# Kernel tuning notes

Hardware: AMD Instinct MI355X
Metric: run time of the kernel (lower is better)

Reference implementation:

```python
import jax, jax.numpy as jnp
import numpy as np

LAYER_START = 4
WIN = 2          # context_window_size (over the LAYER axis)
NORM_EPS = 1e-12 # F.normalize eps
COS_EPS = 1e-8   # cosine_similarity eps


def _alpha_for_k(sf, k, nlay):
    """Alignment/novelty weights for layer k. sf: [B, Ttok, Lay, H].
    Mirrors torch: left = tf[k-w:k] (empty when k<w due to python slicing),
    right = tf[k+1:k+w+1], self row last; QR of window_matrix.T."""
    left = list(range(k - WIN, k)) if k >= WIN else []
    right = list(range(k + 1, min(k + WIN + 1, nlay)))
    rows = left + right + [k]
    m = len(rows)  # 3..5
    W = sf[:, :, jnp.array(rows), :]          # [B,T,m,H]
    A = jnp.swapaxes(W, -1, -2)               # [B,T,H,m]  (window_matrix.T)
    _, R = jnp.linalg.qr(A)                   # reduced: R [B,T,m,m]
    r = R[..., :, -1]                         # [B,T,m]
    Rsub = R[..., :-1, :-1]                   # [B,T,m-1,m-1]
    coln = Rsub / jnp.maximum(jnp.linalg.norm(Rsub, axis=-2, keepdims=True), NORM_EPS)
    row_mean = jnp.mean(coln, axis=-1)        # mean over columns -> [B,T,m-1]
    align = jnp.sum(row_mean * R[..., :-1, -1], axis=-1) / jnp.linalg.norm(r[..., :-1], axis=-1)
    align = 1.0 / (align * m * 2)
    novelty = jnp.abs(r[..., -1]) / jnp.linalg.norm(r, axis=-1)
    return align, novelty


def wk_forward(all_hidden_states, attention_mask):
    # [NL,B,T,H] -> [B, Lay, T, H] after layer_start slice
    emb = jnp.transpose(all_hidden_states, (1, 0, 2, 3))[:, LAYER_START:, :, :]
    B, Lay, T, H = emb.shape
    ntok = T - 1  # attention_mask is all-ones: unmask_num = sum(mask) - 1
    sf = jnp.transpose(emb[:, :, :ntok, :], (0, 2, 1, 3))  # [B,Ttok,Lay,H]
    aligns, novs = [], []
    for k in range(Lay):  # small fixed loop over 9 layers
        a, n = _alpha_for_k(sf, k, Lay)
        aligns.append(a)
        novs.append(n)
    align = jnp.stack(aligns, axis=-1)  # [B,Ttok,Lay]
    nov = jnp.stack(novs, axis=-1)
    align = align / jnp.sum(align, axis=-1, keepdims=True)
    nov = nov / jnp.sum(nov, axis=-1, keepdims=True)
    alpha = align + nov
    alpha = alpha / jnp.sum(alpha, axis=-1, keepdims=True)
    token_emb = jnp.einsum('btl,btlh->bth', alpha, sf)  # unify_token output per token
    # unify_sentence: per-token variance (unbiased) of consecutive-layer cosine sims
    a, b = sf[:, :, 1:, :], sf[:, :, :-1, :]
    num = jnp.sum(a * b, axis=-1)
    den = jnp.maximum(jnp.linalg.norm(a, axis=-1) * jnp.linalg.norm(b, axis=-1), COS_EPS)
    sims = num / den                              # [B,Ttok,Lay-1]
    var_tok = jnp.var(sims, axis=-1, ddof=1)      # torch.var default unbiased
    var_tok = var_tok / jnp.sum(var_tok, axis=-1, keepdims=True)
    return jnp.einsum('bt,bth->bh', var_tok, token_emb)  # [B,H]


def setup_inputs() -> dict:
    key = jax.random.key(0)
    NL, B, T, H = 13, 8, 512, 768
    all_hidden_states = jax.random.normal(key, (NL, B, T, H), dtype=jnp.float32)
    attention_mask = jnp.ones((B, T), dtype=jnp.int32)
    return {"all_hidden_states": all_hidden_states, "attention_mask": attention_mask}


def reference(all_hidden_states, attention_mask):
    return wk_forward(all_hidden_states, attention_mask)
```

## Files before the change

### kernel.cpp

```cpp
#include <hip/hip_runtime.h>
#include <math.h>

#define B_DIM 8
#define T_DIM 512
#define H_DIM 768
#define NTOK 511
#define NLAY 9
#define LAYER_START 4
#define NBAND 35
#define TCHUNK 128

__device__ float g_part[B_DIM * TCHUNK * H_DIM];
__device__ float g_varp[B_DIM * TCHUNK];

#define BOFF(d) ((d)*9 - (d) * ((d)-1) / 2)

template <int CTRL>
__device__ __forceinline__ float dpp_mov(float x) {
  return __builtin_bit_cast(
      float, __builtin_amdgcn_update_dpp(0, __builtin_bit_cast(int, x), CTRL,
                                         0xF, 0xF, true));
}

__device__ __forceinline__ float wave_sum_dpp(float x) {
  x += dpp_mov<0x111>(x);
  x += dpp_mov<0x112>(x);
  x += dpp_mov<0x114>(x);
  x += dpp_mov<0x118>(x);
  x += dpp_mov<0x142>(x);
  x += dpp_mov<0x143>(x);
  return x;
}

__global__ __launch_bounds__(256, 2) void wk_a(const float* __restrict__ ahs) {
  const int chunk = blockIdx.x;
  const int b = blockIdx.y;
  const int wave = threadIdx.x >> 6;
  const int lane = threadIdx.x & 63;
  const int t_raw = chunk * 4 + wave;
  const bool active = (t_raw < NTOK);
  const int t = active ? t_raw : (NTOK - 1);

  __shared__ float sG[4][36];
  __shared__ float lds_out[4][H_DIM];
  __shared__ float lds_var[4];

  const size_t LSTR = (size_t)B_DIM * T_DIM * H_DIM;
  const float* lay0 =
      ahs + (size_t)LAYER_START * LSTR + ((size_t)b * T_DIM + t) * H_DIM;

  float4 v[NLAY][3];
#pragma unroll
  for (int l = 0; l < NLAY; ++l) {
    const float* base = lay0 + (size_t)l * LSTR;
#pragma unroll
    for (int s = 0; s < 3; ++s) {
      v[l][s] = *reinterpret_cast<const float4*>(base + s * 256 + lane * 4);
    }
  }

#pragma unroll
  for (int d = 0; d <= 4; ++d) {
    float gd[NLAY];
#pragma unroll
    for (int i = 0; i + d < NLAY; ++i) {
      float s0 = 0.f;
#pragma unroll
      for (int s = 0; s < 3; ++s) {
        const float4 x = v[i][s], y = v[i + d][s];
        s0 += x.x * y.x + x.y * y.y + x.z * y.z + x.w * y.w;
      }
      gd[i] = s0;
    }
#pragma unroll
    for (int i = 0; i + d < NLAY; ++i) gd[i] = wave_sum_dpp(gd[i]);
    if (lane == 63) {
#pragma unroll
      for (int i = 0; i + d < NLAY; ++i) sG[wave][BOFF(d) + i] = gd[i];
    }
  }
  __builtin_amdgcn_wave_barrier();

  const int k = lane < NLAY ? lane : NLAY - 1;
  const int nl = (k >= 2) ? 2 : 0;
  const int nrr = (NLAY - 1 - k) < 2 ? (NLAY - 1 - k) : 2;
  const int m = nl + nrr + 1;

  auto rowf = [&](int i) -> int {
    return (i < nl) ? (k - 2 + i) : ((i < nl + nrr) ? (k + 1 + i - nl) : k);
  };
  auto GK = [&](int i, int j) -> float {
    int a = rowf(i), c = rowf(j);
    int lo = a < c ? a : c;
    int d = (a < c ? c : a) - lo;
    return sG[wave][d * 9 - d * (d - 1) / 2 + lo];
  };

  float R[5][5];
#pragma unroll
  for (int j = 0; j < 5; ++j)
#pragma unroll
    for (int i = 0; i < 5; ++i) R[i][j] = 0.f;

#pragma unroll
  for (int j = 0; j < 5; ++j) {
    if (j < m) {
#pragma unroll
      for (int i = 0; i < 5; ++i) {
        if (i < j) {
          float s = GK(i, j);
#pragma unroll
          for (int p = 0; p < 4; ++p)
            if (p < i) s -= R[p][i] * R[p][j];
          R[i][j] = s / R[i][i];
        }
      }
      float sjj = GK(j, j);
#pragma unroll
      for (int p = 0; p < 4; ++p)
        if (p < j) sjj -= R[p][j] * R[p][j];
      R[j][j] = sqrtf(fmaxf(sjj, 0.f));
    }
  }

  float r[5];
#pragma unroll
  for (int i = 0; i < 5; ++i)
    r[i] = (m == 3) ? R[i][2] : ((m == 4) ? R[i][3] : R[i][4]);

  float rowmean[4] = {0.f, 0.f, 0.f, 0.f};
#pragma unroll
  for (int j = 0; j < 4; ++j) {
    if (j < m - 1) {
      float cn = 0.f;
#pragma unroll
      for (int i = 0; i < 4; ++i)
        if (i <= j) cn += R[i][j] * R[i][j];
      cn = fmaxf(sqrtf(cn), 1e-12f);
      float inv = 1.f / cn;
#pragma unroll
      for (int i = 0; i < 4; ++i)
        if (i < m - 1) rowmean[i] += R[i][j] * inv;
    }
  }

  const float inv_m1 = 1.f / (float)(m - 1);
  float dotv = 0.f, nrm2 = 0.f;
#pragma unroll
  for (int i = 0; i < 4; ++i) {
    if (i < m - 1) {
      dotv += (rowmean[i] * inv_m1) * r[i];
      nrm2 += r[i] * r[i];
    }
  }
  float align_raw = dotv / sqrtf(nrm2);
  float align_v = 1.f / (align_raw * (float)m * 2.f);
  float rlast = (m == 3) ? r[2] : ((m == 4) ? r[3] : r[4]);
  float nov_v = fabsf(rlast) / sqrtf(nrm2 + rlast * rlast);

  float al[NLAY], nv[NLAY];
  float asum = 0.f, nsum = 0.f;
#pragma unroll
  for (int l = 0; l < NLAY; ++l) {
    al[l] = __shfl(align_v, l, 64);
    nv[l] = __shfl(nov_v, l, 64);
    asum += al[l];
    nsum += nv[l];
  }
  float alpha[NLAY];
  float csum = 0.f;
#pragma unroll
  for (int l = 0; l < NLAY; ++l) {
    alpha[l] = al[l] / asum + nv[l] / nsum;
    csum += alpha[l];
  }
  const float inv_csum = 1.f / csum;

  float sims[NLAY - 1];
  float smean = 0.f;
#pragma unroll
  for (int j = 0; j < NLAY - 1; ++j) {
    float num = sG[wave][BOFF(1) + j];
    float den = fmaxf(sqrtf(sG[wave][j]) * sqrtf(sG[wave][j + 1]), 1e-8f);
    sims[j] = num / den;
    smean += sims[j];
  }
  smean *= (1.f / 8.f);
  float var = 0.f;
#pragma unroll
  for (int j = 0; j < NLAY - 1; ++j) {
    float d = sims[j] - smean;
    var += d * d;
  }
  var *= (1.f / 7.f);
  if (!active) var = 0.f;

  if (lane == 0) lds_var[wave] = var;

  float c[NLAY];
#pragma unroll
  for (int l = 0; l < NLAY; ++l) c[l] = var * alpha[l] * inv_csum;

#pragma unroll
  for (int s = 0; s < 3; ++s) {
    float4 o;
    o.x = 0.f; o.y = 0.f; o.z = 0.f; o.w = 0.f;
#pragma unroll
    for (int l = 0; l < NLAY; ++l) {
      o.x += c[l] * v[l][s].x;
      o.y += c[l] * v[l][s].y;
      o.z += c[l] * v[l][s].z;
      o.w += c[l] * v[l][s].w;
    }
    *reinterpret_cast<float4*>(&lds_out[wave][s * 256 + lane * 4]) = o;
  }
  __syncthreads();

  float* dst = g_part + ((size_t)(b * TCHUNK + chunk)) * H_DIM;
#pragma unroll
  for (int s = 0; s < 3; ++s) {
    int h = s * 256 + threadIdx.x;
    float sum = lds_out[0][h] + lds_out[1][h] + lds_out[2][h] + lds_out[3][h];
    dst[h] = sum;
  }
  if (threadIdx.x == 0) {
    g_varp[b * TCHUNK + chunk] =
        lds_var[0] + lds_var[1] + lds_var[2] + lds_var[3];
  }
}

__global__ __launch_bounds__(256) void wk_r(float* __restrict__ out) {
  const int b = blockIdx.y;
  const int tid = threadIdx.x;
  const int h = blockIdx.x * 256 + tid;

  __shared__ float s_ws[4];
  float vs = (tid < TCHUNK) ? g_varp[b * TCHUNK + tid] : 0.f;
  vs = wave_sum_dpp(vs);
  if ((tid & 63) == 63) s_ws[tid >> 6] = vs;
  __syncthreads();
  const float ssum = s_ws[0] + s_ws[1];

  float acc = 0.f;
#pragma unroll 16
  for (int j = 0; j < TCHUNK; ++j)
    acc += g_part[((size_t)(b * TCHUNK + j)) * H_DIM + h];

  out[b * H_DIM + h] = acc / ssum;
}

extern "C" void kernel_launch(void* const* d_in, const int* in_sizes, int n_in,
                              void* d_out, int out_size, void* d_ws, size_t ws_size,
                              hipStream_t stream) {
  const float* ahs = (const float*)d_in[0];
  float* out = (float*)d_out;
  (void)d_ws; (void)ws_size;

  wk_a<<<dim3(TCHUNK, B_DIM), dim3(256), 0, stream>>>(ahs);
  wk_r<<<dim3(3, B_DIM), dim3(256), 0, stream>>>(out);
}
```

Before: 224.5 us.

## Split each token's hidden dim across two waves to halve per-wave registers

Each token is now handled by a pair of waves, each loading half of the hidden dimension (a float4 plus a float2 per lane per layer). Partial Gram entries are combined through shared memory after a block barrier. Blocks now cover two tokens instead of four, so the grid doubles to 256 chunks and the reduction kernel sums twice as many partials. The aim is lower register pressure and more in-flight memory parallelism, at the cost of a block-wide sync, duplicated QR math in both waves, and more partial-sum traffic.

```diff
diff --git a/kernel.cpp b/kernel.cpp
--- a/kernel.cpp
+++ b/kernel.cpp
@@ -8,10 +8,11 @@
 #define NLAY 9
 #define LAYER_START 4
 #define NBAND 35
-#define TCHUNK 128
-
-__device__ float g_part[B_DIM * TCHUNK * H_DIM];
-__device__ float g_varp[B_DIM * TCHUNK];
+#define CHUNKS 256
+#define HHALF 384
+
+__device__ float g_part[B_DIM * CHUNKS * H_DIM];
+__device__ float g_varp[B_DIM * CHUNKS];
 
 #define BOFF(d) ((d)*9 - (d) * ((d)-1) / 2)
 
@@ -37,26 +38,28 @@
   const int b = blockIdx.y;
   const int wave = threadIdx.x >> 6;
   const int lane = threadIdx.x & 63;
-  const int t_raw = chunk * 4 + wave;
+  const int slot = wave >> 1;
+  const int half = wave & 1;
+  const int pb = wave & ~1;
+  const int t_raw = chunk * 2 + slot;
   const bool active = (t_raw < NTOK);
   const int t = active ? t_raw : (NTOK - 1);
 
   __shared__ float sG[4][36];
-  __shared__ float lds_out[4][H_DIM];
-  __shared__ float lds_var[4];
+  __shared__ float lds_out[2][H_DIM];
+  __shared__ float lds_var[2];
 
   const size_t LSTR = (size_t)B_DIM * T_DIM * H_DIM;
-  const float* lay0 =
-      ahs + (size_t)LAYER_START * LSTR + ((size_t)b * T_DIM + t) * H_DIM;
-
-  float4 v[NLAY][3];
-#pragma unroll
-  for (int l = 0; l < NLAY; ++l) {
-    const float* base = lay0 + (size_t)l * LSTR;
-#pragma unroll
-    for (int s = 0; s < 3; ++s) {
-      v[l][s] = *reinterpret_cast<const float4*>(base + s * 256 + lane * 4);
-    }
+  const float* base0 = ahs + (size_t)LAYER_START * LSTR +
+                       ((size_t)b * T_DIM + t) * H_DIM + half * HHALF;
+
+  float4 v4[NLAY];
+  float2 v2[NLAY];
+#pragma unroll
+  for (int l = 0; l < NLAY; ++l) {
+    const float* base = base0 + (size_t)l * LSTR;
+    v4[l] = *reinterpret_cast<const float4*>(base + lane * 4);
+    v2[l] = *reinterpret_cast<const float2*>(base + 256 + lane * 2);
   }
 
 #pragma unroll
@@ -64,13 +67,10 @@
     float gd[NLAY];
 #pragma unroll
     for (int i = 0; i + d < NLAY; ++i) {
-      float s0 = 0.f;
-#pragma unroll
-      for (int s = 0; s < 3; ++s) {
-        const float4 x = v[i][s], y = v[i + d][s];
-        s0 += x.x * y.x + x.y * y.y + x.z * y.z + x.w * y.w;
-      }
-      gd[i] = s0;
+      const float4 x4 = v4[i], y4 = v4[i + d];
+      const float2 x2 = v2[i], y2 = v2[i + d];
+      gd[i] = x4.x * y4.x + x4.y * y4.y + x4.z * y4.z + x4.w * y4.w +
+              x2.x * y2.x + x2.y * y2.y;
     }
 #pragma unroll
     for (int i = 0; i + d < NLAY; ++i) gd[i] = wave_sum_dpp(gd[i]);
@@ -79,7 +79,9 @@
       for (int i = 0; i + d < NLAY; ++i) sG[wave][BOFF(d) + i] = gd[i];
     }
   }
-  __builtin_amdgcn_wave_barrier();
+  __syncthreads();
+
+  auto SC = [&](int idx) -> float { return sG[pb][idx] + sG[pb + 1][idx]; };
 
   const int k = lane < NLAY ? lane : NLAY - 1;
   const int nl = (k >= 2) ? 2 : 0;
@@ -93,7 +95,7 @@
     int a = rowf(i), c = rowf(j);
     int lo = a < c ? a : c;
     int d = (a < c ? c : a) - lo;
-    return sG[wave][d * 9 - d * (d - 1) / 2 + lo];
+    return SC(d * 9 - d * (d - 1) / 2 + lo);
   };
 
   float R[5][5];
@@ -158,30 +160,27 @@
   float rlast = (m == 3) ? r[2] : ((m == 4) ? r[3] : r[4]);
   float nov_v = fabsf(rlast) / sqrtf(nrm2 + rlast * rlast);
 
-  float al[NLAY], nv[NLAY];
   float asum = 0.f, nsum = 0.f;
 #pragma unroll
   for (int l = 0; l < NLAY; ++l) {
-    al[l] = __shfl(align_v, l, 64);
-    nv[l] = __shfl(nov_v, l, 64);
-    asum += al[l];
-    nsum += nv[l];
-  }
-  float alpha[NLAY];
+    asum += __shfl(align_v, l, 64);
+    nsum += __shfl(nov_v, l, 64);
+  }
+  float c[NLAY];
   float csum = 0.f;
 #pragma unroll
   for (int l = 0; l < NLAY; ++l) {
-    alpha[l] = al[l] / asum + nv[l] / nsum;
-    csum += alpha[l];
-  }
-  const float inv_csum = 1.f / csum;
+    float a = __shfl(align_v, l, 64) / asum + __shfl(nov_v, l, 64) / nsum;
+    c[l] = a;
+    csum += a;
+  }
 
   float sims[NLAY - 1];
   float smean = 0.f;
 #pragma unroll
   for (int j = 0; j < NLAY - 1; ++j) {
-    float num = sG[wave][BOFF(1) + j];
-    float den = fmaxf(sqrtf(sG[wave][j]) * sqrtf(sG[wave][j + 1]), 1e-8f);
+    float num = SC(BOFF(1) + j);
+    float den = fmaxf(sqrtf(SC(j)) * sqrtf(SC(j + 1)), 1e-8f);
     sims[j] = num / den;
     smean += sims[j];
   }
@@ -195,37 +194,38 @@
   var *= (1.f / 7.f);
   if (!active) var = 0.f;
 
-  if (lane == 0) lds_var[wave] = var;
-
-  float c[NLAY];
-#pragma unroll
-  for (int l = 0; l < NLAY; ++l) c[l] = var * alpha[l] * inv_csum;
-
-#pragma unroll
-  for (int s = 0; s < 3; ++s) {
-    float4 o;
-    o.x = 0.f; o.y = 0.f; o.z = 0.f; o.w = 0.f;
-#pragma unroll
-    for (int l = 0; l < NLAY; ++l) {
-      o.x += c[l] * v[l][s].x;
-      o.y += c[l] * v[l][s].y;
-      o.z += c[l] * v[l][s].z;
-      o.w += c[l] * v[l][s].w;
-    }
-    *reinterpret_cast<float4*>(&lds_out[wave][s * 256 + lane * 4]) = o;
-  }
+  if (lane == 0 && half == 0) lds_var[slot] = var;
+
+  const float scale = var / csum;
+#pragma unroll
+  for (int l = 0; l < NLAY; ++l) c[l] *= scale;
+
+  float4 o4;
+  o4.x = 0.f; o4.y = 0.f; o4.z = 0.f; o4.w = 0.f;
+  float2 o2;
+  o2.x = 0.f; o2.y = 0.f;
+#pragma unroll
+  for (int l = 0; l < NLAY; ++l) {
+    o4.x += c[l] * v4[l].x;
+    o4.y += c[l] * v4[l].y;
+    o4.z += c[l] * v4[l].z;
+    o4.w += c[l] * v4[l].w;
+    o2.x += c[l] * v2[l].x;
+    o2.y += c[l] * v2[l].y;
+  }
+  *reinterpret_cast<float4*>(&lds_out[slot][half * HHALF + lane * 4]) = o4;
+  *reinterpret_cast<float2*>(&lds_out[slot][half * HHALF + 256 + lane * 2]) =
+      o2;
   __syncthreads();
 
-  float* dst = g_part + ((size_t)(b * TCHUNK + chunk)) * H_DIM;
+  float* dst = g_part + ((size_t)(b * CHUNKS + chunk)) * H_DIM;
 #pragma unroll
   for (int s = 0; s < 3; ++s) {
     int h = s * 256 + threadIdx.x;
-    float sum = lds_out[0][h] + lds_out[1][h] + lds_out[2][h] + lds_out[3][h];
-    dst[h] = sum;
+    dst[h] = lds_out[0][h] + lds_out[1][h];
   }
   if (threadIdx.x == 0) {
-    g_varp[b * TCHUNK + chunk] =
-        lds_var[0] + lds_var[1] + lds_var[2] + lds_var[3];
+    g_varp[b * CHUNKS + chunk] = lds_var[0] + lds_var[1];
   }
 }
 
@@ -235,16 +235,16 @@
   const int h = blockIdx.x * 256 + tid;
 
   __shared__ float s_ws[4];
-  float vs = (tid < TCHUNK) ? g_varp[b * TCHUNK + tid] : 0.f;
+  float vs = g_varp[b * CHUNKS + tid];
   vs = wave_sum_dpp(vs);
   if ((tid & 63) == 63) s_ws[tid >> 6] = vs;
   __syncthreads();
-  const float ssum = s_ws[0] + s_ws[1];
+  const float ssum = s_ws[0] + s_ws[1] + s_ws[2] + s_ws[3];
 
   float acc = 0.f;
 #pragma unroll 16
-  for (int j = 0; j < TCHUNK; ++j)
-    acc += g_part[((size_t)(b * TCHUNK + j)) * H_DIM + h];
+  for (int j = 0; j < CHUNKS; ++j)
+    acc += g_part[((size_t)(b * CHUNKS + j)) * H_DIM + h];
 
   out[b * H_DIM + h] = acc / ssum;
 }
@@ -256,6 +256,6 @@
   float* out = (float*)d_out;
   (void)d_ws; (void)ws_size;
 
-  wk_a<<<dim3(TCHUNK, B_DIM), dim3(256), 0, stream>>>(ahs);
+  wk_a<<<dim3(CHUNKS, B_DIM), dim3(256), 0, stream>>>(ahs);
   wk_r<<<dim3(3, B_DIM), dim3(256), 0, stream>>>(out);
 }
```

Result: slower. 231.4 us (+3.1%).

## Use one-wave blocks per token and move the cross-token reduction to the final kernel

Applied to the files above, without the earlier changes.

The main kernel now launches one 64-thread block per token instead of 256-thread blocks covering four tokens. It drops the LDS cross-wave sum and __syncthreads, and writes each token's weighted partial vector straight to global memory. Input loads are marked nontemporal. The reduction kernel now uses 1024 threads to sum 511 partials per batch instead of 128. This removes intra-block sync and LDS traffic, but the partial buffer grows about fourfold, adding global write and read traffic for the second kernel.

```diff
diff --git a/kernel.cpp b/kernel.cpp
--- a/kernel.cpp
+++ b/kernel.cpp
@@ -8,10 +8,11 @@
 #define NLAY 9
 #define LAYER_START 4
 #define NBAND 35
-#define TCHUNK 128
-
-__device__ float g_part[B_DIM * TCHUNK * H_DIM];
-__device__ float g_varp[B_DIM * TCHUNK];
+
+typedef float vf4 __attribute__((ext_vector_type(4)));
+
+__device__ float g_part[B_DIM * NTOK * H_DIM];
+__device__ float g_varp[B_DIM * NTOK];
 
 #define BOFF(d) ((d)*9 - (d) * ((d)-1) / 2)
 
@@ -32,30 +33,25 @@
   return x;
 }
 
-__global__ __launch_bounds__(256, 2) void wk_a(const float* __restrict__ ahs) {
-  const int chunk = blockIdx.x;
+__global__ __launch_bounds__(64) void wk_a(const float* __restrict__ ahs) {
+  const int t = blockIdx.x;
   const int b = blockIdx.y;
-  const int wave = threadIdx.x >> 6;
-  const int lane = threadIdx.x & 63;
-  const int t_raw = chunk * 4 + wave;
-  const bool active = (t_raw < NTOK);
-  const int t = active ? t_raw : (NTOK - 1);
-
-  __shared__ float sG[4][36];
-  __shared__ float lds_out[4][H_DIM];
-  __shared__ float lds_var[4];
+  const int lane = threadIdx.x;
+
+  __shared__ float sG[36];
 
   const size_t LSTR = (size_t)B_DIM * T_DIM * H_DIM;
   const float* lay0 =
       ahs + (size_t)LAYER_START * LSTR + ((size_t)b * T_DIM + t) * H_DIM;
 
-  float4 v[NLAY][3];
+  vf4 v[NLAY][3];
 #pragma unroll
   for (int l = 0; l < NLAY; ++l) {
     const float* base = lay0 + (size_t)l * LSTR;
 #pragma unroll
     for (int s = 0; s < 3; ++s) {
-      v[l][s] = *reinterpret_cast<const float4*>(base + s * 256 + lane * 4);
+      v[l][s] = __builtin_nontemporal_load(
+          reinterpret_cast<const vf4*>(base + s * 256 + lane * 4));
     }
   }
 
@@ -67,7 +63,7 @@
       float s0 = 0.f;
 #pragma unroll
       for (int s = 0; s < 3; ++s) {
-        const float4 x = v[i][s], y = v[i + d][s];
+        const vf4 x = v[i][s], y = v[i + d][s];
         s0 += x.x * y.x + x.y * y.y + x.z * y.z + x.w * y.w;
       }
       gd[i] = s0;
@@ -76,7 +72,7 @@
     for (int i = 0; i + d < NLAY; ++i) gd[i] = wave_sum_dpp(gd[i]);
     if (lane == 63) {
 #pragma unroll
-      for (int i = 0; i + d < NLAY; ++i) sG[wave][BOFF(d) + i] = gd[i];
+      for (int i = 0; i + d < NLAY; ++i) sG[BOFF(d) + i] = gd[i];
     }
   }
   __builtin_amdgcn_wave_barrier();
@@ -93,7 +89,7 @@
     int a = rowf(i), c = rowf(j);
     int lo = a < c ? a : c;
     int d = (a < c ? c : a) - lo;
-    return sG[wave][d * 9 - d * (d - 1) / 2 + lo];
+    return sG[d * 9 - d * (d - 1) / 2 + lo];
   };
 
   float R[5][5];
@@ -158,30 +154,27 @@
   float rlast = (m == 3) ? r[2] : ((m == 4) ? r[3] : r[4]);
   float nov_v = fabsf(rlast) / sqrtf(nrm2 + rlast * rlast);
 
-  float al[NLAY], nv[NLAY];
   float asum = 0.f, nsum = 0.f;
 #pragma unroll
   for (int l = 0; l < NLAY; ++l) {
-    al[l] = __shfl(align_v, l, 64);
-    nv[l] = __shfl(nov_v, l, 64);
-    asum += al[l];
-    nsum += nv[l];
-  }
-  float alpha[NLAY];
+    asum += __shfl(align_v, l, 64);
+    nsum += __shfl(nov_v, l, 64);
+  }
+  float c[NLAY];
   float csum = 0.f;
 #pragma unroll
   for (int l = 0; l < NLAY; ++l) {
-    alpha[l] = al[l] / asum + nv[l] / nsum;
-    csum += alpha[l];
-  }
-  const float inv_csum = 1.f / csum;
+    float a = __shfl(align_v, l, 64) / asum + __shfl(nov_v, l, 64) / nsum;
+    c[l] = a;
+    csum += a;
+  }
 
   float sims[NLAY - 1];
   float smean = 0.f;
 #pragma unroll
   for (int j = 0; j < NLAY - 1; ++j) {
-    float num = sG[wave][BOFF(1) + j];
-    float den = fmaxf(sqrtf(sG[wave][j]) * sqrtf(sG[wave][j + 1]), 1e-8f);
+    float num = sG[BOFF(1) + j];
+    float den = fmaxf(sqrtf(sG[j]) * sqrtf(sG[j + 1]), 1e-8f);
     sims[j] = num / den;
     smean += sims[j];
   }
@@ -193,18 +186,15 @@
     var += d * d;
   }
   var *= (1.f / 7.f);
-  if (!active) var = 0.f;
-
-  if (lane == 0) lds_var[wave] = var;
-
-  float c[NLAY];
-#pragma unroll
-  for (int l = 0; l < NLAY; ++l) c[l] = var * alpha[l] * inv_csum;
-
+
+  const float scale = var / csum;
+#pragma unroll
+  for (int l = 0; l < NLAY; ++l) c[l] *= scale;
+
+  float* dst = g_part + ((size_t)(b * NTOK + t)) * H_DIM;
 #pragma unroll
   for (int s = 0; s < 3; ++s) {
-    float4 o;
-    o.x = 0.f; o.y = 0.f; o.z = 0.f; o.w = 0.f;
+    vf4 o = {0.f, 0.f, 0.f, 0.f};
 #pragma unroll
     for (int l = 0; l < NLAY; ++l) {
       o.x += c[l] * v[l][s].x;
@@ -212,41 +202,38 @@
       o.z += c[l] * v[l][s].z;
       o.w += c[l] * v[l][s].w;
     }
-    *reinterpret_cast<float4*>(&lds_out[wave][s * 256 + lane * 4]) = o;
-  }
-  __syncthreads();
-
-  float* dst = g_part + ((size_t)(b * TCHUNK + chunk)) * H_DIM;
-#pragma unroll
-  for (int s = 0; s < 3; ++s) {
-    int h = s * 256 + threadIdx.x;
-    float sum = lds_out[0][h] + lds_out[1][h] + lds_out[2][h] + lds_out[3][h];
-    dst[h] = sum;
-  }
-  if (threadIdx.x == 0) {
-    g_varp[b * TCHUNK + chunk] =
-        lds_var[0] + lds_var[1] + lds_var[2] + lds_var[3];
-  }
-}
-
-__global__ __launch_bounds__(256) void wk_r(float* __restrict__ out) {
+    *reinterpret_cast<vf4*>(dst + s * 256 + lane * 4) = o;
+  }
+  if (lane == 0) g_varp[b * NTOK + t] = var;
+}
+
+__global__ __launch_bounds__(1024) void wk_r(float* __restrict__ out) {
   const int b = blockIdx.y;
-  const int tid = threadIdx.x;
+  const int grp = threadIdx.x >> 8;
+  const int tid = threadIdx.x & 255;
   const int h = blockIdx.x * 256 + tid;
 
-  __shared__ float s_ws[4];
-  float vs = (tid < TCHUNK) ? g_varp[b * TCHUNK + tid] : 0.f;
+  __shared__ float s_ws[16];
+  __shared__ float s_acc[4][256];
+
+  float vs = (threadIdx.x < NTOK) ? g_varp[b * NTOK + threadIdx.x] : 0.f;
   vs = wave_sum_dpp(vs);
-  if ((tid & 63) == 63) s_ws[tid >> 6] = vs;
-  __syncthreads();
-  const float ssum = s_ws[0] + s_ws[1];
+  if ((threadIdx.x & 63) == 63) s_ws[threadIdx.x >> 6] = vs;
 
   float acc = 0.f;
 #pragma unroll 16
-  for (int j = 0; j < TCHUNK; ++j)
-    acc += g_part[((size_t)(b * TCHUNK + j)) * H_DIM + h];
-
-  out[b * H_DIM + h] = acc / ssum;
+  for (int j = grp; j < NTOK; j += 4)
+    acc += g_part[((size_t)(b * NTOK + j)) * H_DIM + h];
+  s_acc[grp][tid] = acc;
+  __syncthreads();
+
+  if (grp == 0) {
+    float ssum = 0.f;
+#pragma unroll
+    for (int w = 0; w < 16; ++w) ssum += s_ws[w];
+    float tot = s_acc[0][tid] + s_acc[1][tid] + s_acc[2][tid] + s_acc[3][tid];
+    out[b * H_DIM + h] = tot / ssum;
+  }
 }
 
 extern "C" void kernel_launch(void* const* d_in, const int* in_sizes, int n_in,
@@ -256,6 +243,6 @@
   float* out = (float*)d_out;
   (void)d_ws; (void)ws_size;
 
-  wk_a<<<dim3(TCHUNK, B_DIM), dim3(256), 0, stream>>>(ahs);
-  wk_r<<<dim3(3, B_DIM), dim3(256), 0, stream>>>(out);
-}
+  wk_a<<<dim3(NTOK, B_DIM), dim3(64), 0, stream>>>(ahs);
+  wk_r<<<dim3(3, B_DIM), dim3(1024), 0, stream>>>(out);
+}
```

Measured after the change: 234.4 us. +4.4%, slower.
